# Kernel optimization log

Measured on AMD Instinct MI355X. Metric: run time of the kernel, lower is better.

Reference implementation:

```python
import jax, jax.numpy as jnp
import numpy as np

H_GRID = 24
W_GRID = 24
NUM_HEADS = 3
FEAT_DIM = 192
HEAD_DIM = FEAT_DIM // NUM_HEADS  # 64
SCALE = HEAD_DIM ** -0.5
LN_EPS = 1e-5


def _positional():
    # matches get_positional_encodings with intrinsics=None; depends only on grid
    ys = jnp.linspace(-1.0, 1.0, H_GRID)
    xs = jnp.linspace(-1.0, 1.0, W_GRID)
    p3 = jnp.tile(ys, W_GRID)            # [N]
    p4 = jnp.repeat(xs, H_GRID)          # [N]
    p2 = p3 * p4
    p1 = p4 * p4
    p0 = p3 * p3
    return jnp.stack([p0, p1, p2, p3, p4, jnp.ones_like(p0)], axis=1)  # [N, 6]


def _layernorm(x, w, b):
    mu = jnp.mean(x, axis=-1, keepdims=True)
    var = jnp.mean((x - mu) ** 2, axis=-1, keepdims=True)
    return (x - mu) / jnp.sqrt(var + LN_EPS) * w + b


def _qkv_heads(x, qkv_w):
    # x: [B, N, C] -> q,k,v each [B, H, N, hd]
    B, N, _ = x.shape
    qkv = x @ qkv_w.T                                    # [B, N, 3*F]
    qkv = qkv.reshape(B, N, 3, NUM_HEADS, HEAD_DIM)
    qkv = jnp.transpose(qkv, (2, 0, 3, 1, 4))            # [3, B, H, N, hd]
    return qkv[0], qkv[1], qkv[2]


def _dual_softmax(attn):
    return jax.nn.softmax(attn, axis=-1) * jax.nn.softmax(attn, axis=-2)


def setup_inputs() -> dict:
    key = jax.random.key(0)
    ks = jax.random.split(key, 4)
    B, C = 64, 256
    in_dim, out_dim = C, 512
    dim_size = 2 * NUM_HEADS * (HEAD_DIM + 6) * (HEAD_DIM + 6)  # 29400
    return {
        "x1": jax.random.normal(ks[0], (B, C, H_GRID, W_GRID), jnp.float32),
        "x2": jax.random.normal(ks[1], (B, C, H_GRID, W_GRID), jnp.float32),
        "ln_w": jnp.ones((in_dim,), jnp.float32),
        "ln_b": jnp.zeros((in_dim,), jnp.float32),
        "qkv_w": jax.random.normal(ks[2], (3 * FEAT_DIM, in_dim), jnp.float32) * (in_dim ** -0.5),
        "proj_w": jax.random.normal(ks[3], (out_dim, dim_size), jnp.float32) * (dim_size ** -0.5),
        "proj_b": jnp.zeros((out_dim,), jnp.float32),
    }


def reference(x1, x2, ln_w, ln_b, qkv_w, proj_w, proj_b):
    B, C, h, w = x1.shape
    N = h * w
    x1t = _layernorm(x1.reshape(B, C, N).transpose(0, 2, 1), ln_w, ln_b)  # [B, N, C]
    x2t = _layernorm(x2.reshape(B, C, N).transpose(0, 2, 1), ln_w, ln_b)

    q1, k1, v1 = _qkv_heads(x1t, qkv_w)
    q2, k2, v2 = _qkv_heads(x2t, qkv_w)

    attn_1 = jnp.einsum("bhnd,bhmd->bhnm", q2, k1) * SCALE
    attn_2 = jnp.einsum("bhnd,bhmd->bhnm", q1, k2) * SCALE
    af1 = _dual_softmax(attn_1)
    af2 = _dual_softmax(attn_2)

    pos = jnp.broadcast_to(_positional(), (B, NUM_HEADS, N, 6))
    v1p = jnp.concatenate([v1, pos], axis=-1)  # [B, H, N, hd+6]
    v2p = jnp.concatenate([v2, pos], axis=-1)

    f1 = jnp.einsum("bhnd,bhnm,bhme->bhde", v1p, af1, v1p)  # [B, H, hd+6, hd+6]
    f2 = jnp.einsum("bhnd,bhnm,bhme->bhde", v2p, af2, v2p)

    feat = jnp.concatenate([f1.reshape(B, -1), f2.reshape(B, -1)], axis=-1)
    return jax.nn.relu(feat @ proj_w.T + proj_b)
```

## Files before the change

### kernel.cpp

```cpp
#include <hip/hip_runtime.h>

#define NSEQ 576
#define CDIM 256
#define HEADS 3
#define HD 64
#define FEAT 192
#define QKVF 576
#define QK_F 384
#define VP 70
#define BHN 192
#define DIMSZ 29400

typedef __attribute__((ext_vector_type(8))) _Float16 half8;
typedef __attribute__((ext_vector_type(4))) _Float16 half4;
typedef __attribute__((ext_vector_type(4))) float f32x4;

#define MFMA16(A,B,C) __builtin_amdgcn_mfma_f32_16x16x32_f16(A,B,C,0,0,0)

__device__ __forceinline__ float posval(int n, int pe){
  int yi = n % 24, xi = n / 24;
  float py = (float)yi * (2.0f/23.0f) - 1.0f;
  float px = (float)xi * (2.0f/23.0f) - 1.0f;
  switch(pe){
    case 0: return py*py;
    case 1: return px*px;
    case 2: return py*px;
    case 3: return py;
    case 4: return px;
    default: return 1.0f;
  }
}

template<int LD>
__device__ __forceinline__ half8 fragT(const _Float16 (*s)[LD], int row, int dbase){
  half4 a = *(const half4*)&s[row][dbase];
  half4 b = *(const half4*)&s[row][dbase + 16];
  return __builtin_shufflevector(a, b, 0, 1, 2, 3, 4, 5, 6, 7);
}

__device__ __forceinline__ void stage_copy64(const _Float16* __restrict__ src, int rstr,
                                             _Float16 (*d)[72], int t){
  #pragma unroll
  for (int k2 = 0; k2 < 2; ++k2){
    int idx = t + 256 * k2;
    int row = idx >> 3, c = (idx & 7) << 3;
    half8 v = *(const half8*)(src + (size_t)row * rstr + c);
    *(half4*)&d[row][c]     = (half4){v[0], v[1], v[2], v[3]};
    *(half4*)&d[row][c + 4] = (half4){v[4], v[5], v[6], v[7]};
  }
}

__device__ __forceinline__ int rotIdx(int row, int c16){
  return row * 64 + ((((c16) + row) & 7) << 3);
}

__global__ __launch_bounds__(192) void k_ln_stats(const float* __restrict__ x1, const float* __restrict__ x2,
                                                  float* __restrict__ mu, float* __restrict__ rstd){
  int idx = blockIdx.x;
  int i2 = idx / 192;
  int rem = idx % 192;
  int b = rem / 3, ng = rem % 3;
  int n = ng * 192 + threadIdx.x;
  const float* x = i2 ? x2 : x1;
  const float* xb = x + (size_t)b * CDIM * NSEQ + n;
  float s = 0.f, sq = 0.f;
  for (int c = 0; c < CDIM; ++c){
    float v = xb[(size_t)c * NSEQ];
    s += v; sq += v * v;
  }
  float m = s * (1.0f/256.0f);
  float var = sq * (1.0f/256.0f) - m * m;
  int o = (i2 * 64 + b) * NSEQ + n;
  mu[o] = m;
  rstd[o] = rsqrtf(var + 1e-5f);
}

__global__ __launch_bounds__(256) void k_w_repack(const float* __restrict__ qkvw,
                                                  _Float16* __restrict__ wrh, _Float16* __restrict__ wrl){
  int idx = blockIdx.x * 256 + threadIdx.x;
  if (idx >= 18432) return;
  int fi = idx & 63;
  int r = idx >> 6;
  int hi = r & 3; r >>= 2;
  int kc = r & 1; r >>= 1;
  int cb = r & 3; r >>= 2;
  int ft = r;
  int f = ft * 64 + fi;
  int cbase = cb * 64 + kc * 32 + hi * 4;
  const float* src = qkvw + (size_t)f * CDIM + cbase;
  float4 a = *(const float4*)src;
  float4 b = *(const float4*)(src + 16);
  float vv[8] = {a.x, a.y, a.z, a.w, b.x, b.y, b.z, b.w};
  half8 h, l;
  #pragma unroll
  for (int j = 0; j < 8; ++j){
    _Float16 hh = (_Float16)vv[j];
    h[j] = hh;
    l[j] = (_Float16)(vv[j] - (float)hh);
  }
  *(half8*)(wrh + (size_t)idx * 8) = h;
  *(half8*)(wrl + (size_t)idx * 8) = l;
}

__global__ __launch_bounds__(256) void k_qkv_gemm_mfma(const float* __restrict__ x1, const float* __restrict__ x2,
                                                       const float* __restrict__ mu, const float* __restrict__ rstd,
                                                       const float* __restrict__ lnw, const float* __restrict__ lnb,
                                                       const _Float16* __restrict__ wrh, const _Float16* __restrict__ wrl,
                                                       _Float16* __restrict__ qh, _Float16* __restrict__ ql,
                                                       _Float16* __restrict__ vpTh, _Float16* __restrict__ vpTl){
  int wg = (blockIdx.x & 7) * 1296 + (blockIdx.x >> 3);
  int ft = wg % 9;
  int mt = wg / 9;
  int ibn = mt * 64;
  int i2 = ibn / (64 * NSEQ);
  int bn = ibn % (64 * NSEQ);
  int b  = bn / NSEQ;
  int n0 = bn % NSEQ;
  const float* x = i2 ? x2 : x1;
  const float* xb = x + (size_t)b * CDIM * NSEQ + n0;
  __shared__ __align__(16) _Float16 Xh[64][68];
  __shared__ __align__(16) _Float16 Xl[64][68];
  __shared__ float smu[64], srstd[64], slnw[256], slnb[256];
  int t = threadIdx.x;
  int w = t >> 6, lane = t & 63, tx = lane & 15, hi = lane >> 4;
  if (t < 64){ smu[t] = mu[ibn + t]; srstd[t] = rstd[ibn + t]; }
  slnw[t] = lnw[t]; slnb[t] = lnb[t];

  f32x4 acc[4];
  #pragma unroll
  for (int s = 0; s < 4; ++s) acc[s] = (f32x4){0.f, 0.f, 0.f, 0.f};

  int nA = t & 63, cg = t >> 6;
  int lchunk = hi * 64 + w * 16 + tx;
  for (int c0 = 0; c0 < CDIM; c0 += 64){
    int cb = c0 >> 6;
    __syncthreads();
    float mun = smu[nA], rsn = srstd[nA];
    #pragma unroll
    for (int rr = 0; rr < 16; ++rr){
      int c = cg * 16 + rr;
      float v = xb[(size_t)(c0 + c) * NSEQ + nA];
      float xv = (v - mun) * rsn * slnw[c0 + c] + slnb[c0 + c];
      _Float16 hh = (_Float16)xv;
      Xh[nA][c] = hh;
      Xl[nA][c] = (_Float16)(xv - (float)hh);
    }
    __syncthreads();
    #pragma unroll
    for (int kc = 0; kc < 2; ++kc){
      size_t wo = ((size_t)((ft * 4 + cb) * 2 + kc) * 256 + lchunk) * 8;
      half8 wh = *(const half8*)(wrh + wo);
      half8 wl = *(const half8*)(wrl + wo);
      #pragma unroll
      for (int s = 0; s < 4; ++s){
        half8 xh = fragT<68>(Xh, s * 16 + tx, kc * 32 + hi * 4);
        half8 xl = fragT<68>(Xl, s * 16 + tx, kc * 32 + hi * 4);
        acc[s] = MFMA16(xh, wh, acc[s]);
        acc[s] = MFMA16(xl, wh, acc[s]);
        acc[s] = MFMA16(xh, wl, acc[s]);
      }
    }
  }
  if (ft < 6){
    #pragma unroll
    for (int s = 0; s < 4; ++s)
      #pragma unroll
      for (int rr = 0; rr < 4; ++rr){
        float v = acc[s][rr];
        _Float16 hh = (_Float16)v;
        size_t o = (size_t)(ibn + s * 16 + hi * 4 + rr) * QK_F + ft * 64 + w * 16 + tx;
        qh[o] = hh;
        ql[o] = (_Float16)(v - (float)hh);
      }
  } else {
    __syncthreads();
    #pragma unroll
    for (int s = 0; s < 4; ++s)
      #pragma unroll
      for (int rr = 0; rr < 4; ++rr){
        float v = acc[s][rr];
        _Float16 hh = (_Float16)v;
        Xh[s * 16 + hi * 4 + rr][w * 16 + tx] = hh;
        Xl[s * 16 + hi * 4 + rr][w * 16 + tx] = (_Float16)(v - (float)hh);
      }
    __syncthreads();
    int mbg = i2 * 192 + b * 3 + (ft - 6);
    #pragma unroll
    for (int it = 0; it < 16; ++it){
      int d = (t >> 6) + it * 4;
      int n2 = t & 63;
      size_t o = ((size_t)mbg * 80 + d) * NSEQ + n0 + n2;
      vpTh[o] = Xh[n2][d];
      vpTl[o] = Xl[n2][d];
    }
  }
}

__global__ __launch_bounds__(256) void k_pos_fill(_Float16* __restrict__ vpTh, _Float16* __restrict__ vpTl){
  int idx = blockIdx.x * 256 + threadIdx.x;
  if (idx >= 384 * 16 * NSEQ) return;
  int n = idx % NSEQ;
  int r = idx / NSEQ;
  int row = 64 + (r & 15);
  int mb = r >> 4;
  float v = 0.f;
  int pe = row - 64;
  if (pe < 6) v = posval(n, pe);
  _Float16 hh = (_Float16)v;
  size_t o = ((size_t)mb * 80 + row) * NSEQ + n;
  vpTh[o] = hh;
  vpTl[o] = (_Float16)(v - (float)hh);
}

__global__ __launch_bounds__(256) void k_attn_stats_mfma(const _Float16* __restrict__ qh, const _Float16* __restrict__ ql,
                                                         float* __restrict__ rs, float* __restrict__ cs_part){
  int wg = (blockIdx.x & 7) * 432 + (blockIdx.x >> 3);
  int map = wg / (BHN * 9);
  int r   = wg % (BHN * 9);
  int bh = r / 9, nt = r % 9;
  int b = bh / 3, h = bh % 3;
  int qi = 1 - map, ki = map;
  int mb = map * BHN + bh;
  const _Float16* qbh = qh + (size_t)((qi * 64 + b) * NSEQ) * QK_F + h * HD;
  const _Float16* qbl = ql + (size_t)((qi * 64 + b) * NSEQ) * QK_F + h * HD;
  const _Float16* kbh = qh + (size_t)((ki * 64 + b) * NSEQ) * QK_F + FEAT + h * HD;
  const _Float16* kbl = ql + (size_t)((ki * 64 + b) * NSEQ) * QK_F + FEAT + h * HD;
  int n0 = nt * 64;
  __shared__ __align__(16) _Float16 Kh[64 * 64];
  __shared__ __align__(16) _Float16 Kl[64 * 64];
  __shared__ float rsLds[4][64];
  int t = threadIdx.x;
  int w = t >> 6, lane = t & 63, tx = lane & 15, hi = lane >> 4;

  for (int idx = t; idx < 1024; idx += 256){
    int a = idx >> 9, rc = idx & 511, row = rc >> 3, c16 = rc & 7;
    const _Float16* src = a ? qbl : qbh;
    _Float16* dst = a ? Kl : Kh;
    *(half8*)(dst + rotIdx(row, c16)) = *(const half8*)(src + (size_t)(n0 + row) * QK_F + c16 * 8);
  }
  __syncthreads();
  half8 qAh[4][2], qAl[4][2];
  #pragma unroll
  for (int s = 0; s < 4; ++s)
    #pragma unroll
    for (int kc = 0; kc < 2; ++kc){
      qAh[s][kc] = *(half8*)(Kh + rotIdx(s * 16 + tx, kc * 4 + hi));
      qAl[s][kc] = *(half8*)(Kl + rotIdx(s * 16 + tx, kc * 4 + hi));
    }

  float rsum[4][4] = {};
  for (int mt = 0; mt < 9; ++mt){
    int m0 = mt * 64;
    __syncthreads();
    for (int idx = t; idx < 1024; idx += 256){
      int a = idx >> 9, rc = idx & 511, row = rc >> 3, c16 = rc & 7;
      const _Float16* src = a ? kbl : kbh;
      _Float16* dst = a ? Kl : Kh;
      *(half8*)(dst + rotIdx(row, c16)) = *(const half8*)(src + (size_t)(m0 + row) * QK_F + c16 * 8);
    }
    __syncthreads();
    f32x4 acc[4];
    #pragma unroll
    for (int s = 0; s < 4; ++s) acc[s] = (f32x4){0.f, 0.f, 0.f, 0.f};
    #pragma unroll
    for (int kc = 0; kc < 2; ++kc){
      half8 kb8 = *(half8*)(Kh + rotIdx(w * 16 + tx, kc * 4 + hi));
      half8 kl8 = *(half8*)(Kl + rotIdx(w * 16 + tx, kc * 4 + hi));
      #pragma unroll
      for (int s = 0; s < 4; ++s){
        acc[s] = MFMA16(qAh[s][kc], kb8, acc[s]);
        acc[s] = MFMA16(qAl[s][kc], kb8, acc[s]);
        acc[s] = MFMA16(qAh[s][kc], kl8, acc[s]);
      }
    }
    float csum = 0.f;
    #pragma unroll
    for (int s = 0; s < 4; ++s)
      #pragma unroll
      for (int rr = 0; rr < 4; ++rr){
        float e = __expf(acc[s][rr] * 0.125f);
        rsum[s][rr] += e;
        csum += e;
      }
    csum += __shfl_xor(csum, 16);
    csum += __shfl_xor(csum, 32);
    if (lane < 16)
      cs_part[((size_t)mb * 9 + nt) * NSEQ + m0 + w * 16 + tx] = csum;
  }
  #pragma unroll
  for (int s = 0; s < 4; ++s)
    #pragma unroll
    for (int rr = 0; rr < 4; ++rr){
      float v = rsum[s][rr];
      v += __shfl_xor(v, 1);
      v += __shfl_xor(v, 2);
      v += __shfl_xor(v, 4);
      v += __shfl_xor(v, 8);
      if (tx == 0) rsLds[w][s * 16 + hi * 4 + rr] = v;
    }
  __syncthreads();
  if (t < 64)
    rs[(size_t)mb * NSEQ + n0 + t] = rsLds[0][t] + rsLds[1][t] + rsLds[2][t] + rsLds[3][t];
}

__global__ __launch_bounds__(256) void k_cs_reduce(const float* __restrict__ cs_part, float* __restrict__ cs){
  int tid = blockIdx.x * 256 + threadIdx.x;
  if (tid >= 2 * BHN * NSEQ) return;
  int mb = tid / NSEQ, m = tid % NSEQ;
  float s = 0.f;
  #pragma unroll
  for (int p = 0; p < 9; ++p)
    s += cs_part[((size_t)mb * 9 + p) * NSEQ + m];
  cs[tid] = s;
}

__global__ __launch_bounds__(256) void k_apply_mfma(const _Float16* __restrict__ qh, const _Float16* __restrict__ ql,
                                                    const _Float16* __restrict__ vpTh, const _Float16* __restrict__ vpTl,
                                                    const float* __restrict__ rs, const float* __restrict__ cs,
                                                    _Float16* __restrict__ tTh, _Float16* __restrict__ tTl, int map){
  int wg = (blockIdx.x & 7) * 216 + (blockIdx.x >> 3);
  int bh = wg / 9, nt = wg % 9;
  int b = bh / 3, h = bh % 3;
  int qi = 1 - map, ki = map;
  int mb = map * BHN + bh;
  const _Float16* qbh = qh + (size_t)((qi * 64 + b) * NSEQ) * QK_F + h * HD;
  const _Float16* qbl = ql + (size_t)((qi * 64 + b) * NSEQ) * QK_F + h * HD;
  const _Float16* kbh = qh + (size_t)((ki * 64 + b) * NSEQ) * QK_F + FEAT + h * HD;
  const _Float16* kbl = ql + (size_t)((ki * 64 + b) * NSEQ) * QK_F + FEAT + h * HD;
  const _Float16* vTh = vpTh + (size_t)mb * 80 * NSEQ;
  const _Float16* vTl = vpTl + (size_t)mb * 80 * NSEQ;
  int n0 = nt * 64;
  __shared__ __align__(16) _Float16 Ash[64][72];
  __shared__ __align__(16) _Float16 Asl[64][72];
  __shared__ __align__(16) _Float16 Vth[80][72];
  __shared__ __align__(16) _Float16 Vtl[80][72];
  __shared__ float cinv[64];
  int t = threadIdx.x;
  int w = t >> 6, lane = t & 63, tx = lane & 15, hi = lane >> 4;

  stage_copy64(qbh + (size_t)n0 * QK_F, QK_F, Ash, t);
  stage_copy64(qbl + (size_t)n0 * QK_F, QK_F, Asl, t);
  __syncthreads();
  half8 qB0h = fragT<72>(Ash, w * 16 + tx, 0 + hi * 4);
  half8 qB1h = fragT<72>(Ash, w * 16 + tx, 32 + hi * 4);
  half8 qB0l = fragT<72>(Asl, w * 16 + tx, 0 + hi * 4);
  half8 qB1l = fragT<72>(Asl, w * 16 + tx, 32 + hi * 4);
  float rinv = 1.0f / rs[(size_t)mb * NSEQ + n0 + w * 16 + tx];

  f32x4 tacc[5];
  #pragma unroll
  for (int et = 0; et < 5; ++et) tacc[et] = (f32x4){0.f, 0.f, 0.f, 0.f};

  for (int mt = 0; mt < 9; ++mt){
    int m0 = mt * 64;
    __syncthreads();
    stage_copy64(kbh + (size_t)m0 * QK_F, QK_F, Ash, t);
    stage_copy64(kbl + (size_t)m0 * QK_F, QK_F, Asl, t);
    #pragma unroll
    for (int k2 = 0; k2 < 3; ++k2){
      int idx = t + 256 * k2;
      if (idx < 640){
        int row = idx >> 3, c = (idx & 7) << 3;
        half8 v1 = *(const half8*)(vTh + (size_t)row * NSEQ + m0 + c);
        *(half4*)&Vth[row][c]     = (half4){v1[0], v1[1], v1[2], v1[3]};
        *(half4*)&Vth[row][c + 4] = (half4){v1[4], v1[5], v1[6], v1[7]};
        half8 v2 = *(const half8*)(vTl + (size_t)row * NSEQ + m0 + c);
        *(half4*)&Vtl[row][c]     = (half4){v2[0], v2[1], v2[2], v2[3]};
        *(half4*)&Vtl[row][c + 4] = (half4){v2[4], v2[5], v2[6], v2[7]};
      }
    }
    if (t < 64) cinv[t] = 1.0f / cs[(size_t)mb * NSEQ + m0 + t];
    __syncthreads();

    f32x4 acc[4];
    #pragma unroll
    for (int s = 0; s < 4; ++s) acc[s] = (f32x4){0.f, 0.f, 0.f, 0.f};
    #pragma unroll
    for (int s = 0; s < 4; ++s){
      half8 kh0 = fragT<72>(Ash, s * 16 + tx, 0 + hi * 4);
      half8 kl0 = fragT<72>(Asl, s * 16 + tx, 0 + hi * 4);
      half8 kh1 = fragT<72>(Ash, s * 16 + tx, 32 + hi * 4);
      half8 kl1 = fragT<72>(Asl, s * 16 + tx, 32 + hi * 4);
      acc[s] = MFMA16(kh0, qB0h, acc[s]);
      acc[s] = MFMA16(kl0, qB0h, acc[s]);
      acc[s] = MFMA16(kh0, qB0l, acc[s]);
      acc[s] = MFMA16(kh1, qB1h, acc[s]);
      acc[s] = MFMA16(kl1, qB1h, acc[s]);
      acc[s] = MFMA16(kh1, qB1l, acc[s]);
    }
    half8 bph[2], bpl[2];
    #pragma unroll
    for (int s = 0; s < 4; ++s){
      #pragma unroll
      for (int rr = 0; rr < 4; ++rr){
        float af = __expf(acc[s][rr] * 0.25f) * rinv * cinv[s * 16 + hi * 4 + rr];
        _Float16 hh = (_Float16)af;
        bph[s >> 1][(s & 1) * 4 + rr] = hh;
        bpl[s >> 1][(s & 1) * 4 + rr] = (_Float16)(af - (float)hh);
      }
    }
    #pragma unroll
    for (int et = 0; et < 5; ++et)
      #pragma unroll
      for (int mc = 0; mc < 2; ++mc){
        half8 vhf = fragT<72>(Vth, et * 16 + tx, mc * 32 + hi * 4);
        half8 vlf = fragT<72>(Vtl, et * 16 + tx, mc * 32 + hi * 4);
        tacc[et] = MFMA16(vhf, bph[mc], tacc[et]);
        tacc[et] = MFMA16(vhf, bpl[mc], tacc[et]);
        tacc[et] = MFMA16(vlf, bph[mc], tacc[et]);
      }
  }
  #pragma unroll
  for (int et = 0; et < 5; ++et)
    #pragma unroll
    for (int rr = 0; rr < 4; ++rr){
      int e = et * 16 + hi * 4 + rr;
      float v = tacc[et][rr];
      _Float16 hh = (_Float16)v;
      size_t o = ((size_t)bh * 80 + e) * NSEQ + n0 + w * 16 + tx;
      tTh[o] = hh;
      tTl[o] = (_Float16)(v - (float)hh);
    }
}

__global__ __launch_bounds__(256) void k_f_gemm_mfma(const _Float16* __restrict__ vpTh, const _Float16* __restrict__ vpTl,
                                                     const _Float16* __restrict__ tTh, const _Float16* __restrict__ tTl,
                                                     float* __restrict__ featT3, int map){
  int wg = blockIdx.x;
  int mbL = wg / 3, part = wg % 3;
  int b = mbL / 3, h = mbL % 3;
  __shared__ __align__(16) _Float16 Ah[80][40], Al[80][40], Bh[80][40], Bl[80][40];
  int t = threadIdx.x;
  int w4 = t >> 6, lane = t & 63, tx = lane & 15, hi = lane >> 4;
  const _Float16* Abh = vpTh + (size_t)(map * BHN + mbL) * 80 * NSEQ;
  const _Float16* Abl = vpTl + (size_t)(map * BHN + mbL) * 80 * NSEQ;
  const _Float16* Bbh = tTh + (size_t)mbL * 80 * NSEQ;
  const _Float16* Bbl = tTl + (size_t)mbL * 80 * NSEQ;
  f32x4 acc[7];
  #pragma unroll
  for (int j = 0; j < 7; ++j) acc[j] = (f32x4){0.f, 0.f, 0.f, 0.f};

  for (int kc = part * 6; kc < part * 6 + 6; ++kc){
    int c0 = kc * 32;
    __syncthreads();
    #pragma unroll
    for (int k2 = 0; k2 < 2; ++k2){
      int idx = t + 256 * k2;
      if (idx < 320){
        int row = idx >> 2, cc = (idx & 3) << 3;
        *(half8*)&Ah[row][cc] = *(const half8*)(Abh + (size_t)row * NSEQ + c0 + cc);
        *(half8*)&Al[row][cc] = *(const half8*)(Abl + (size_t)row * NSEQ + c0 + cc);
        *(half8*)&Bh[row][cc] = *(const half8*)(Bbh + (size_t)row * NSEQ + c0 + cc);
        *(half8*)&Bl[row][cc] = *(const half8*)(Bbl + (size_t)row * NSEQ + c0 + cc);
      }
    }
    __syncthreads();
    #pragma unroll
    for (int j = 0; j < 7; ++j){
      int ti = w4 + 4 * j;
      if (ti < 25){
        int db = ti / 5, eb = ti % 5;
        half8 ah = *(const half8*)&Ah[db * 16 + tx][hi * 8];
        half8 al = *(const half8*)&Al[db * 16 + tx][hi * 8];
        half8 bh = *(const half8*)&Bh[eb * 16 + tx][hi * 8];
        half8 bl = *(const half8*)&Bl[eb * 16 + tx][hi * 8];
        acc[j] = MFMA16(ah, bh, acc[j]);
        acc[j] = MFMA16(al, bh, acc[j]);
        acc[j] = MFMA16(ah, bl, acc[j]);
      }
    }
  }
  #pragma unroll
  for (int j = 0; j < 7; ++j){
    int ti = w4 + 4 * j;
    if (ti < 25){
      int db = ti / 5, eb = ti % 5;
      #pragma unroll
      for (int rr = 0; rr < 4; ++rr){
        int d = db * 16 + hi * 4 + rr, e = eb * 16 + tx;
        if (d < VP && e < VP)
          featT3[(size_t)part * 1881600 + (size_t)(map * 14700 + h * 4900 + d * VP + e) * 64 + b] = acc[j][rr];
      }
    }
  }
}

__global__ __launch_bounds__(256) void k_feat_reduce(const float* __restrict__ featT3, float* __restrict__ featT){
  int gid = blockIdx.x * 256 + threadIdx.x;
  if (gid >= DIMSZ * 64) return;
  featT[gid] = featT3[gid] + featT3[1881600 + gid] + featT3[2 * 1881600 + gid];
}

__global__ __launch_bounds__(256) void k_proj_gemm(const float* __restrict__ featT, const float* __restrict__ pw,
                                                   float* __restrict__ p){
  int ot = blockIdx.x & 7;
  int s  = blockIdx.x >> 3;
  int o0 = ot * 64;
  int kbase = s * 300;
  __shared__ __align__(16) float As[20][72];
  __shared__ __align__(16) float Bs[20][72];
  int t = threadIdx.x, tx = t & 15, ty = t >> 4;
  float acc[4][4] = {};
  for (int kt = 0; kt < 15; ++kt){
    int k0 = kbase + kt * 20;
    __syncthreads();
    #pragma unroll
    for (int r = 0; r < 5; ++r){
      int idx = t + 256 * r;
      int bb = idx & 63, kk = idx >> 6;
      As[kk][bb] = featT[(size_t)(k0 + kk) * 64 + bb];
      int ko = idx % 20, oo = idx / 20;
      Bs[ko][oo] = pw[(size_t)(o0 + oo) * DIMSZ + k0 + ko];
    }
    __syncthreads();
    #pragma unroll
    for (int k = 0; k < 20; ++k){
      float4 a4 = *(const float4*)&As[k][ty * 4];
      float4 b4 = *(const float4*)&Bs[k][tx * 4];
      float aa[4] = {a4.x, a4.y, a4.z, a4.w};
      float bb[4] = {b4.x, b4.y, b4.z, b4.w};
      #pragma unroll
      for (int i = 0; i < 4; ++i)
        #pragma unroll
        for (int j = 0; j < 4; ++j)
          acc[i][j] += aa[i] * bb[j];
    }
  }
  int slice = s * 8 + ot;
  #pragma unroll
  for (int i = 0; i < 4; ++i){
    float4 st = make_float4(acc[i][0], acc[i][1], acc[i][2], acc[i][3]);
    *(float4*)&p[(size_t)slice * 4096 + (ty * 4 + i) * 64 + tx * 4] = st;
  }
}

__global__ __launch_bounds__(256) void k_finalize(const float* __restrict__ p, const float* __restrict__ pb,
                                                  float* __restrict__ out){
  int gid = blockIdx.x * 256 + threadIdx.x;
  int o = gid & 511, b = gid >> 9;
  int ot = o >> 6, lo = o & 63;
  float s = pb[o];
  for (int s2 = 0; s2 < 98; ++s2)
    s += p[(size_t)(s2 * 8 + ot) * 4096 + b * 64 + lo];
  out[gid] = fmaxf(s, 0.0f);
}

extern "C" void kernel_launch(void* const* d_in, const int* in_sizes, int n_in,
                              void* d_out, int out_size, void* d_ws, size_t ws_size,
                              hipStream_t stream) {
  const float* x1   = (const float*)d_in[0];
  const float* x2   = (const float*)d_in[1];
  const float* lnw  = (const float*)d_in[2];
  const float* lnb  = (const float*)d_in[3];
  const float* qkvw = (const float*)d_in[4];
  const float* pw   = (const float*)d_in[5];
  const float* pb   = (const float*)d_in[6];
  float* out = (float*)d_out;

  float* w = (float*)d_ws;
  float*     mu      = w;
  float*     rstd    = w + 73728;
  _Float16*  qh      = (_Float16*)(w + 147456);
  _Float16*  ql      = (_Float16*)(w + 14303232);
  _Float16*  vpTh    = (_Float16*)(w + 28459008);
  _Float16*  vpTl    = (_Float16*)(w + 37306368);
  _Float16*  tTh     = (_Float16*)(w + 46153728);
  _Float16*  tTl     = (_Float16*)(w + 50577408);
  float*     cs_part = w + 55001088;
  float*     featT   = w + 55001088;
  float*     rs      = w + 56991744;
  float*     cs      = w + 57212928;
  float*     featT3  = w + 57434112;
  float*     p       = w + 57434112;
  _Float16*  wrh     = (_Float16*)(w + 60645376);
  _Float16*  wrl     = (_Float16*)(w + 60719104);

  k_ln_stats<<<384, 192, 0, stream>>>(x1, x2, mu, rstd);
  k_w_repack<<<72, 256, 0, stream>>>(qkvw, wrh, wrl);
  k_qkv_gemm_mfma<<<10368, 256, 0, stream>>>(x1, x2, mu, rstd, lnw, lnb, wrh, wrl, qh, ql, vpTh, vpTl);
  k_pos_fill<<<13824, 256, 0, stream>>>(vpTh, vpTl);
  k_attn_stats_mfma<<<3456, 256, 0, stream>>>(qh, ql, rs, cs_part);
  k_cs_reduce<<<864, 256, 0, stream>>>(cs_part, cs);
  for (int map = 0; map < 2; ++map){
    k_apply_mfma<<<1728, 256, 0, stream>>>(qh, ql, vpTh, vpTl, rs, cs, tTh, tTl, map);
    k_f_gemm_mfma<<<576, 256, 0, stream>>>(vpTh, vpTl, tTh, tTl, featT3, map);
  }
  k_feat_reduce<<<7350, 256, 0, stream>>>(featT3, featT);
  k_proj_gemm<<<784, 256, 0, stream>>>(featT, pw, p);
  k_finalize<<<128, 256, 0, stream>>>(p, pb, out);
}
```

Measured before the change: 707.8 us.

## Double-buffer K tiles in attention stats and prefetch K into registers

The stats kernel now keeps two LDS buffers for K, stages the next K tile while MFMAs run on the current one, and needs only one barrier per iteration. The second attention kernel loads the next K tile from global memory into registers before the compute loop, then writes it to LDS at the start of the following iteration. Both aim to hide global load latency behind MFMA work. The cost is double the LDS for the stats kernel and extra registers for the prefetch, which may lower occupancy.

```diff
diff --git a/kernel.cpp b/kernel.cpp
--- a/kernel.cpp
+++ b/kernel.cpp
@@ -226,17 +226,21 @@
   const _Float16* kbh = qh + (size_t)((ki * 64 + b) * NSEQ) * QK_F + FEAT + h * HD;
   const _Float16* kbl = ql + (size_t)((ki * 64 + b) * NSEQ) * QK_F + FEAT + h * HD;
   int n0 = nt * 64;
-  __shared__ __align__(16) _Float16 Kh[64 * 64];
-  __shared__ __align__(16) _Float16 Kl[64 * 64];
+  __shared__ __align__(16) _Float16 Kh[2][64 * 64];
+  __shared__ __align__(16) _Float16 Kl[2][64 * 64];
   __shared__ float rsLds[4][64];
   int t = threadIdx.x;
   int w = t >> 6, lane = t & 63, tx = lane & 15, hi = lane >> 4;
 
-  for (int idx = t; idx < 1024; idx += 256){
-    int a = idx >> 9, rc = idx & 511, row = rc >> 3, c16 = rc & 7;
-    const _Float16* src = a ? qbl : qbh;
-    _Float16* dst = a ? Kl : Kh;
-    *(half8*)(dst + rotIdx(row, c16)) = *(const half8*)(src + (size_t)(n0 + row) * QK_F + c16 * 8);
+  for (int idx = t; idx < 2048; idx += 256){
+    int tile = idx >> 10;
+    int hl   = (idx >> 9) & 1;
+    int rc   = idx & 511;
+    int row = rc >> 3, c16 = rc & 7;
+    const _Float16* src = tile ? (hl ? qbl : qbh) : (hl ? kbl : kbh);
+    int srow = tile ? (n0 + row) : row;
+    _Float16* dst = (hl ? &Kl[tile][0] : &Kh[tile][0]);
+    *(half8*)(dst + rotIdx(row, c16)) = *(const half8*)(src + (size_t)srow * QK_F + c16 * 8);
   }
   __syncthreads();
   half8 qAh[4][2], qAl[4][2];
@@ -244,28 +248,33 @@
   for (int s = 0; s < 4; ++s)
     #pragma unroll
     for (int kc = 0; kc < 2; ++kc){
-      qAh[s][kc] = *(half8*)(Kh + rotIdx(s * 16 + tx, kc * 4 + hi));
-      qAl[s][kc] = *(half8*)(Kl + rotIdx(s * 16 + tx, kc * 4 + hi));
-    }
-
-  float rsum[4][4] = {};
-  for (int mt = 0; mt < 9; ++mt){
-    int m0 = mt * 64;
-    __syncthreads();
+      qAh[s][kc] = *(half8*)(&Kh[1][0] + rotIdx(s * 16 + tx, kc * 4 + hi));
+      qAl[s][kc] = *(half8*)(&Kl[1][0] + rotIdx(s * 16 + tx, kc * 4 + hi));
+    }
+  __syncthreads();
+
+  auto stageK = [&](int mt2, int bufi){
+    int m0 = mt2 * 64;
     for (int idx = t; idx < 1024; idx += 256){
       int a = idx >> 9, rc = idx & 511, row = rc >> 3, c16 = rc & 7;
       const _Float16* src = a ? kbl : kbh;
-      _Float16* dst = a ? Kl : Kh;
+      _Float16* dst = a ? &Kl[bufi][0] : &Kh[bufi][0];
       *(half8*)(dst + rotIdx(row, c16)) = *(const half8*)(src + (size_t)(m0 + row) * QK_F + c16 * 8);
     }
-    __syncthreads();
+  };
+
+  float rsum[4][4] = {};
+  for (int mt = 0; mt < 9; ++mt){
+    int cur = mt & 1;
+    int m0 = mt * 64;
+    if (mt < 8) stageK(mt + 1, cur ^ 1);
     f32x4 acc[4];
     #pragma unroll
     for (int s = 0; s < 4; ++s) acc[s] = (f32x4){0.f, 0.f, 0.f, 0.f};
     #pragma unroll
     for (int kc = 0; kc < 2; ++kc){
-      half8 kb8 = *(half8*)(Kh + rotIdx(w * 16 + tx, kc * 4 + hi));
-      half8 kl8 = *(half8*)(Kl + rotIdx(w * 16 + tx, kc * 4 + hi));
+      half8 kb8 = *(half8*)(&Kh[cur][0] + rotIdx(w * 16 + tx, kc * 4 + hi));
+      half8 kl8 = *(half8*)(&Kl[cur][0] + rotIdx(w * 16 + tx, kc * 4 + hi));
       #pragma unroll
       for (int s = 0; s < 4; ++s){
         acc[s] = MFMA16(qAh[s][kc], kb8, acc[s]);
@@ -286,6 +295,7 @@
     csum += __shfl_xor(csum, 32);
     if (lane < 16)
       cs_part[((size_t)mb * 9 + nt) * NSEQ + m0 + w * 16 + tx] = csum;
+    __syncthreads();
   }
   #pragma unroll
   for (int s = 0; s < 4; ++s)
@@ -347,6 +357,19 @@
   half8 qB1l = fragT<72>(Asl, w * 16 + tx, 32 + hi * 4);
   float rinv = 1.0f / rs[(size_t)mb * NSEQ + n0 + w * 16 + tx];
 
+  half8 kPh[2], kPl[2];
+  auto loadK = [&](int mt2){
+    int m0 = mt2 * 64;
+    #pragma unroll
+    for (int k2 = 0; k2 < 2; ++k2){
+      int idx = t + 256 * k2;
+      int row = idx >> 3, c = (idx & 7) << 3;
+      kPh[k2] = *(const half8*)(kbh + (size_t)(m0 + row) * QK_F + c);
+      kPl[k2] = *(const half8*)(kbl + (size_t)(m0 + row) * QK_F + c);
+    }
+  };
+  loadK(0);
+
   f32x4 tacc[5];
   #pragma unroll
   for (int et = 0; et < 5; ++et) tacc[et] = (f32x4){0.f, 0.f, 0.f, 0.f};
@@ -354,8 +377,16 @@
   for (int mt = 0; mt < 9; ++mt){
     int m0 = mt * 64;
     __syncthreads();
-    stage_copy64(kbh + (size_t)m0 * QK_F, QK_F, Ash, t);
-    stage_copy64(kbl + (size_t)m0 * QK_F, QK_F, Asl, t);
+    #pragma unroll
+    for (int k2 = 0; k2 < 2; ++k2){
+      int idx = t + 256 * k2;
+      int row = idx >> 3, c = (idx & 7) << 3;
+      half8 vh = kPh[k2], vl = kPl[k2];
+      *(half4*)&Ash[row][c]     = (half4){vh[0], vh[1], vh[2], vh[3]};
+      *(half4*)&Ash[row][c + 4] = (half4){vh[4], vh[5], vh[6], vh[7]};
+      *(half4*)&Asl[row][c]     = (half4){vl[0], vl[1], vl[2], vl[3]};
+      *(half4*)&Asl[row][c + 4] = (half4){vl[4], vl[5], vl[6], vl[7]};
+    }
     #pragma unroll
     for (int k2 = 0; k2 < 3; ++k2){
       int idx = t + 256 * k2;
@@ -371,6 +402,7 @@
     }
     if (t < 64) cinv[t] = 1.0f / cs[(size_t)mb * NSEQ + m0 + t];
     __syncthreads();
+    if (mt < 8) loadK(mt + 1);
 
     f32x4 acc[4];
     #pragma unroll
```

Result: faster. 691.1 us (-2.4%).
